# Kernel tuning notes

Hardware: AMD Instinct MI355X
Metric: run time of the kernel (lower is better)

Reference implementation:

```python
import jax, jax.numpy as jnp
import numpy as np

B, S, CA, CS, CZ, H, L, N = 1, 1024, 768, 384, 64, 16, 2, 2
C = CA // H  # head dim = 48


def setup_inputs():
    key = jax.random.key(0)
    ks = iter(jax.random.split(key, 40))

    def w(shape, scale=0.02):
        return jax.random.normal(next(ks), shape, jnp.float32) * scale

    return dict(
        a=jax.random.normal(next(ks), (B, S, CA), jnp.float32),
        s=jax.random.normal(next(ks), (B, S, CS), jnp.float32),
        z=jax.random.normal(next(ks), (B, S, S, CZ), jnp.float32),
        attn_sn_w=jnp.ones((L, CS), jnp.float32),
        attn_pb_w=w((L, CA, CS)), attn_pb_b=jnp.zeros((L, CA), jnp.float32),
        attn_pnb_w=w((L, CA, CS)),
        pair_w=jnp.ones((L, CZ), jnp.float32), pair_b=jnp.zeros((L, CZ), jnp.float32),
        q_w=w((L, CA, CA)), q_b=jnp.zeros((L, CA), jnp.float32),
        kvg_w=w((L, 3 * CA, CA)),
        bias_w=w((L, H, CZ)), bias_b=jnp.zeros((L, H), jnp.float32),
        ao_w=w((L, CA, CA)),
        out_w=w((L, CA, CS)), out_b=jnp.full((L, CA), -2.0, jnp.float32),
        tr_sn_w=jnp.ones((L, CS), jnp.float32),
        tr_pb_w=w((L, CA, CS)), tr_pb_b=jnp.zeros((L, CA), jnp.float32),
        tr_pnb_w=w((L, CA, CS)),
        tr_a_w=w((L, 2 * N * CA, CA)),
        tr_s_w=w((L, CA, CS)), tr_s_b=jnp.full((L, CA), -2.0, jnp.float32),
        tr_b_w=w((L, CA, N * CA)),
    )


def _ln(x, w=None, b=None, eps=1e-5):
    m = jnp.mean(x, -1, keepdims=True)
    v = jnp.mean(jnp.square(x - m), -1, keepdims=True)
    y = (x - m) * jax.lax.rsqrt(v + eps)
    if w is not None:
        y = y * w
    if b is not None:
        y = y + b
    return y


def _adaln(a, s, sn_w, pb_w, pb_b, pnb_w):
    an = _ln(a)        # LayerNorm, no affine
    sn = _ln(s, sn_w)  # LayerNorm, weight only (bias=False)
    # NOTE: sigmoid wraps the ENTIRE expression, as in the torch source.
    return jax.nn.sigmoid((sn @ pb_w.T + pb_b) * an + sn @ pnb_w.T)


def _forward(a, s, z, attn_sn_w, attn_pb_w, attn_pb_b, attn_pnb_w,
             pair_w, pair_b, q_w, q_b, kvg_w, bias_w, bias_b, ao_w,
             out_w, out_b, tr_sn_w, tr_pb_w, tr_pb_b, tr_pnb_w,
             tr_a_w, tr_s_w, tr_s_b, tr_b_w):
    for l in range(L):
        # ---- AttentionPairBias (beta = 0, s is not None) ----
        a2 = _adaln(a, s, attn_sn_w[l], attn_pb_w[l], attn_pb_b[l], attn_pnb_w[l])
        # torch uses a raw .reshape((B, H, S, c)) with NO transpose -> replicate exactly
        q = (a2 @ q_w[l].T + q_b[l]).reshape(B, H, S, C)
        kvg = (a2 @ kvg_w[l].T).reshape(B, H, S, 3 * C)
        k, v, g = jnp.split(kvg, 3, axis=-1)
        bmat = (_ln(z, pair_w[l], pair_b[l]) @ bias_w[l].T + bias_b[l]).reshape(B, H, S, S)
        scores = jnp.einsum('bhic,bhjc->bhji', q, k) / C + bmat  # divide by c, NOT sqrt(c)
        A = jax.nn.softmax(scores, axis=-1)
        o = jnp.einsum('bhij,bhic->bhjc', A, v)
        attn = (jax.nn.sigmoid(g) * o).reshape(B, S, CA) @ ao_w[l].T
        attn = jax.nn.sigmoid(s @ out_w[l].T + out_b[l]) * attn
        # ---- ConditionedTransitionBlock ----
        a3 = _adaln(a, s, tr_sn_w[l], tr_pb_w[l], tr_pb_b[l], tr_pnb_w[l])
        h1, h2 = jnp.split(a3 @ tr_a_w[l].T, 2, axis=-1)
        bb = jax.nn.silu(h1) * h2
        tr = jax.nn.sigmoid((s @ tr_s_w[l].T + tr_s_b[l]) * (bb @ tr_b_w[l].T))
        a = attn + tr
    return a


def reference(a, s, z, attn_sn_w, attn_pb_w, attn_pb_b, attn_pnb_w,
              pair_w, pair_b, q_w, q_b, kvg_w, bias_w, bias_b, ao_w,
              out_w, out_b, tr_sn_w, tr_pb_w, tr_pb_b, tr_pnb_w,
              tr_a_w, tr_s_w, tr_s_b, tr_b_w):
    return _forward(a, s, z, attn_sn_w, attn_pb_w, attn_pb_b, attn_pnb_w,
                    pair_w, pair_b, q_w, q_b, kvg_w, bias_w, bias_b, ao_w,
                    out_w, out_b, tr_sn_w, tr_pb_w, tr_pb_b, tr_pnb_w,
                    tr_a_w, tr_s_w, tr_s_b, tr_b_w)
```

## Files before the change

kernel.cpp:

```cpp
#include <hip/hip_runtime.h>
#include <hip/hip_bf16.h>
#include <hip/hip_fp16.h>

typedef long long i64;
typedef unsigned short u16;
typedef __attribute__((ext_vector_type(8))) short short8;
typedef __attribute__((ext_vector_type(8))) _Float16 half8;
typedef __attribute__((ext_vector_type(4))) float f32x4;

__device__ __forceinline__ float sigf(float x){ return 1.f/(1.f + __expf(-x)); }
__device__ __forceinline__ u16 f2bu(float v){
  union{ __hip_bfloat16 h; u16 u; } cv; cv.h = __float2bfloat16(v); return cv.u;
}
__device__ __forceinline__ u16 f2hu(float v){
  union{ _Float16 h; u16 u; } cv; cv.h = (_Float16)v; return cv.u;
}
__device__ __forceinline__ float h2f(u16 u){
  union{ u16 u; _Float16 h; } cv; cv.u = u; return (float)cv.h;
}

__global__ void f2b(const float* __restrict__ in, u16* __restrict__ outp, long n){
  long i = ((long)blockIdx.x*256 + threadIdx.x)*4;
  if (i < n){
    float4 v = *(const float4*)(in + i);
    outp[i]   = f2bu(v.x); outp[i+1] = f2bu(v.y);
    outp[i+2] = f2bu(v.z); outp[i+3] = f2bu(v.w);
  }
}

__global__ void f2b_wpool(const float* __restrict__ w0, const float* __restrict__ w1,
                          const float* __restrict__ w2, const float* __restrict__ w3,
                          const float* __restrict__ w4, const float* __restrict__ w5,
                          const float* __restrict__ w6, const float* __restrict__ w7,
                          const float* __restrict__ w8, const float* __restrict__ w9,
                          const float* __restrict__ w10, u16* __restrict__ pool){
  long i = ((long)blockIdx.x*256 + threadIdx.x)*4;
  if (i >= 8257536) return;
  const float* src; long rel;
  if      (i <  294912){ src=w0;  rel=i; }
  else if (i <  589824){ src=w1;  rel=i-294912; }
  else if (i < 1179648){ src=w2;  rel=i-589824; }
  else if (i < 2949120){ src=w3;  rel=i-1179648; }
  else if (i < 3538944){ src=w4;  rel=i-2949120; }
  else if (i < 3833856){ src=w5;  rel=i-3538944; }
  else if (i < 4128768){ src=w6;  rel=i-3833856; }
  else if (i < 4423680){ src=w7;  rel=i-4128768; }
  else if (i < 4718592){ src=w8;  rel=i-4423680; }
  else if (i < 7077888){ src=w9;  rel=i-4718592; }
  else                 { src=w10; rel=i-7077888; }
  float4 v = *(const float4*)(src + rel);
  pool[i]   = f2bu(v.x); pool[i+1] = f2bu(v.y);
  pool[i+2] = f2bu(v.z); pool[i+3] = f2bu(v.w);
}

__global__ __launch_bounds__(256) void ln_rows(const float* __restrict__ x,
                                               float* __restrict__ y, int D){
  long base = (long)blockIdx.x * D;
  int t = threadIdx.x;
  float s = 0.f, ss = 0.f;
  for (int i = t; i < D; i += 256){ float v = x[base+i]; s += v; ss += v*v; }
  __shared__ float r0[256], r1[256];
  r0[t] = s; r1[t] = ss; __syncthreads();
  for (int off = 128; off > 0; off >>= 1){
    if (t < off){ r0[t] += r0[t+off]; r1[t] += r1[t+off]; }
    __syncthreads();
  }
  float mean = r0[0]/D;
  float var  = r1[0]/D - mean*mean;
  float rstd = rsqrtf(var + 1e-5f);
  for (int i = t; i < D; i += 256) y[base+i] = (x[base+i]-mean)*rstd;
}

__global__ void scale2(const float* __restrict__ SN0, const float* __restrict__ w_at,
                       const float* __restrict__ w_tr, u16* __restrict__ y){
  long i = (long)blockIdx.x*256 + threadIdx.x;
  if (i < 786432){
    long tt = i/768, c = i%768;
    float v = (c < 384) ? SN0[tt*384+c]*w_at[c] : SN0[tt*384+c-384]*w_tr[c-384];
    y[i] = f2bu(v);
  }
}

__global__ void adaln2(const float* __restrict__ Pf, const float* __restrict__ AN,
                       const float* __restrict__ b, u16* __restrict__ outb){
  long i = (long)blockIdx.x*256 + threadIdx.x;
  if (i < 786432){
    long tt = i/768, c = i%768;
    float p1 = Pf[tt*1536 + c] + b[c];
    float p2 = Pf[tt*1536 + 768 + c];
    outb[i] = f2bu(sigf(p1*AN[i] + p2));
  }
}

__global__ void catbias(const float* __restrict__ ob, const float* __restrict__ tb,
                        float* __restrict__ g){
  int i = blockIdx.x*256 + threadIdx.x;
  if (i < 3072){
    int l = i/1536, c = i%1536;
    g[i] = (c < 768) ? ob[l*768+c] : tb[l*768+c-768];
  }
}

__global__ void zprep(const float* __restrict__ pw, const float* __restrict__ pb,
                      const float* __restrict__ bw, const float* __restrict__ bb,
                      u16* __restrict__ cwh, float* __restrict__ cb){
  int i = blockIdx.x*256 + threadIdx.x;
  if (i < 2048){
    int l = i/1024, c = i%64;
    cwh[i] = f2hu(pw[l*64+c]*bw[i]);
  } else if (i < 2080){
    int t = i - 2048;
    int l = t/16, mm = t%16;
    float acc = bb[l*16+mm];
    for (int c = 0; c < 64; c++) acc += pb[l*64+c]*bw[l*1024+mm*64+c];
    cb[t] = acc;
  }
}

__global__ __launch_bounds__(256) void zln_mfma(const float* __restrict__ z,
    const u16* __restrict__ Bw,
    const float* __restrict__ cb,
    u16* __restrict__ Zp){
  __shared__ __align__(16) u16 Asm[256*72];
  __shared__ __align__(16) u16 Bsm[32*72];
  int t = threadIdx.x;
  i64 p0 = (i64)blockIdx.x*256;
  if (t < 64){
    int row = t >> 1, half = t & 1;
    const uint4* src = (const uint4*)(Bw + row*64 + half*32);
    uint4* dst = (uint4*)&Bsm[row*72 + half*32];
    dst[0]=src[0]; dst[1]=src[1]; dst[2]=src[2]; dst[3]=src[3];
  }
  int sub = t & 15, rbase = t >> 4;
  const float* zb = z + p0*64;
#pragma unroll
  for (int it = 0; it < 16; it++){
    int row = it*16 + rbase;
    float4 v = *(const float4*)(zb + (i64)row*64 + sub*4);
    float s  = v.x+v.y+v.z+v.w;
    float ss = v.x*v.x+v.y*v.y+v.z*v.z+v.w*v.w;
#pragma unroll
    for (int mk = 1; mk < 16; mk <<= 1){
      s  += __shfl_xor(s,  mk);
      ss += __shfl_xor(ss, mk);
    }
    float mean = s*(1.f/64.f);
    float var  = ss*(1.f/64.f) - mean*mean;
    float r = rsqrtf(var + 1e-5f);
    unsigned int lo = (unsigned int)f2hu((v.x-mean)*r) | ((unsigned int)f2hu((v.y-mean)*r) << 16);
    unsigned int hi = (unsigned int)f2hu((v.z-mean)*r) | ((unsigned int)f2hu((v.w-mean)*r) << 16);
    *(uint2*)&Asm[row*72 + sub*4] = make_uint2(lo, hi);
  }
  __syncthreads();
  int lane = t & 63, wv = t >> 6, la = lane & 15, quad = lane >> 4;
  f32x4 acc[4][2] = {};
#pragma unroll
  for (int kc = 0; kc < 2; kc++){
    half8 af[4], bf[2];
#pragma unroll
    for (int i = 0; i < 4; i++)
      af[i] = *(const half8*)&Asm[(64*wv + 16*i + la)*72 + kc*32 + quad*8];
#pragma unroll
    for (int j = 0; j < 2; j++)
      bf[j] = *(const half8*)&Bsm[(16*j + la)*72 + kc*32 + quad*8];
#pragma unroll
    for (int i = 0; i < 4; i++)
#pragma unroll
      for (int j = 0; j < 2; j++)
        acc[i][j] = __builtin_amdgcn_mfma_f32_16x16x32_f16(af[i], bf[j], acc[i][j], 0,0,0);
  }
  __syncthreads();
#pragma unroll
  for (int i = 0; i < 4; i++)
#pragma unroll
   for (int j = 0; j < 2; j++)
#pragma unroll
    for (int rr = 0; rr < 4; rr++){
      int row = 64*wv + 16*i + quad*4 + rr;
      int gn = 16*j + la;
      Asm[row*72 + gn] = f2hu(acc[i][j][rr] + cb[gn]);
    }
  __syncthreads();
  uint4* o0 = (uint4*)(Zp + (p0 + t)*16);
  uint4* o1 = (uint4*)(Zp + 16777216 + (p0 + t)*16);
  o0[0] = *(uint4*)&Asm[t*72];
  o0[1] = *(uint4*)&Asm[t*72 + 8];
  o1[0] = *(uint4*)&Asm[t*72 + 16];
  o1[1] = *(uint4*)&Asm[t*72 + 24];
}

__global__ __launch_bounds__(256) void rowstat(const float* __restrict__ sc,
                                               float2* __restrict__ st){
  long base = (long)blockIdx.x * 1024;
  const float4* row = (const float4*)(sc + base);
  int t = threadIdx.x;
  float4 v = row[t];
  float mx = fmaxf(fmaxf(v.x,v.y), fmaxf(v.z,v.w));
  for (int off = 32; off > 0; off >>= 1) mx = fmaxf(mx, __shfl_down(mx, off));
  __shared__ float sm[4], ssum[4];
  int wv = t >> 6, ln = t & 63;
  if (ln == 0) sm[wv] = mx;
  __syncthreads();
  mx = fmaxf(fmaxf(sm[0],sm[1]), fmaxf(sm[2],sm[3]));
  float s = __expf(v.x-mx)+__expf(v.y-mx)+__expf(v.z-mx)+__expf(v.w-mx);
  for (int off = 32; off > 0; off >>= 1) s += __shfl_down(s, off);
  if (ln == 0) ssum[wv] = s;
  __syncthreads();
  if (t == 0) st[blockIdx.x] = make_float2(mx, 1.f/(ssum[0]+ssum[1]+ssum[2]+ssum[3]));
}

__global__ __launch_bounds__(256) void vtrans(const float* __restrict__ kvg,
                                              u16* __restrict__ vt){
  int h = blockIdx.x, x0 = blockIdx.y*64;
  __shared__ u16 tile[48][65];
  int t = threadIdx.x;
  for (int idx = t; idx < 64*48; idx += 256){
    int xx = idx/48, c = idx%48;
    tile[c][xx] = f2hu(kvg[(i64)h*147456 + (i64)(x0+xx)*144 + 48 + c]);
  }
  __syncthreads();
  for (int idx = t; idx < 48*64; idx += 256){
    int c = idx>>6, xx = idx&63;
    vt[(i64)h*49152 + (i64)c*1024 + x0 + xx] = tile[c][xx];
  }
}

__global__ __launch_bounds__(256) void av_gemm(
    const float* __restrict__ P,
    const float2* __restrict__ st,
    const u16* __restrict__ Vt,
    const float* __restrict__ kvg,
    u16* __restrict__ Ob)
{
  __shared__ __align__(16) u16 Asm[64*40];
  __shared__ __align__(16) u16 Bsm[64*40];
  int t = threadIdx.x;
  int h = blockIdx.z;
  int m0 = blockIdx.y*64;
  const float* Pp = P + (i64)h*1048576;
  const float2* stp = st + (i64)h*1024;
  const u16* Vp = Vt + (i64)h*49152;
  int lane = t & 63, wv = t >> 6;
  int la = lane & 15, quad = lane >> 4;
  int moff = (wv >> 1)*32, noff = (wv & 1)*32;
  int mcol = t & 63;
  int kr0  = (t >> 6)*2;
  int srow = t >> 2, skc = (t & 3)*8;
  f32x4 acc[2][2] = {{{0.f,0.f,0.f,0.f},{0.f,0.f,0.f,0.f}},
                     {{0.f,0.f,0.f,0.f},{0.f,0.f,0.f,0.f}}};
  float va[4], vb[4];
  float2 sa[4], sb[4];
  uint4 bv;
#pragma unroll
  for (int q = 0; q < 4; q++){
    int kk = kr0 + q*8;
    sa[q] = stp[kk]; sb[q] = stp[kk+1];
    va[q] = Pp[(i64)kk*1024 + m0 + mcol];
    vb[q] = Pp[(i64)(kk+1)*1024 + m0 + mcol];
  }
  bv = make_uint4(0,0,0,0);
  if (srow < 48) bv = *(const uint4*)(Vp + (i64)srow*1024 + skc);
  for (int it = 0; it < 32; it++){
#pragma unroll
    for (int q = 0; q < 4; q++){
      int kk = kr0 + q*8;
      unsigned int pa = f2hu(__expf(va[q] - sa[q].x) * sa[q].y);
      unsigned int pb = f2hu(__expf(vb[q] - sb[q].x) * sb[q].y);
      *(unsigned int*)&Asm[mcol*40 + kk] = pa | (pb << 16);
    }
    *(uint4*)&Bsm[srow*40 + skc] = bv;
    __syncthreads();
    if (it < 31){
      int k0 = (it+1)*32;
#pragma unroll
      for (int q = 0; q < 4; q++){
        int kk = kr0 + q*8;
        sa[q] = stp[k0+kk]; sb[q] = stp[k0+kk+1];
        va[q] = Pp[(i64)(k0+kk)*1024 + m0 + mcol];
        vb[q] = Pp[(i64)(k0+kk+1)*1024 + m0 + mcol];
      }
      bv = make_uint4(0,0,0,0);
      if (srow < 48) bv = *(const uint4*)(Vp + (i64)srow*1024 + k0 + skc);
    }
    half8 af0 = *(const half8*)&Asm[(moff      + la)*40 + quad*8];
    half8 af1 = *(const half8*)&Asm[(moff + 16 + la)*40 + quad*8];
    half8 bf0 = *(const half8*)&Bsm[(noff      + la)*40 + quad*8];
    half8 bf1 = *(const half8*)&Bsm[(noff + 16 + la)*40 + quad*8];
    acc[0][0] = __builtin_amdgcn_mfma_f32_16x16x32_f16(af0, bf0, acc[0][0], 0,0,0);
    acc[0][1] = __builtin_amdgcn_mfma_f32_16x16x32_f16(af0, bf1, acc[0][1], 0,0,0);
    acc[1][0] = __builtin_amdgcn_mfma_f32_16x16x32_f16(af1, bf0, acc[1][0], 0,0,0);
    acc[1][1] = __builtin_amdgcn_mfma_f32_16x16x32_f16(af1, bf1, acc[1][1], 0,0,0);
    __syncthreads();
  }
#pragma unroll
  for (int i = 0; i < 2; i++)
#pragma unroll
   for (int j = 0; j < 2; j++)
#pragma unroll
    for (int r = 0; r < 4; r++){
      int gm = m0 + moff + 16*i + quad*4 + r;
      int gn = noff + 16*j + la;
      if (gn < 48){
        float g = kvg[(i64)h*147456 + (i64)gm*144 + 96 + gn];
        float v = sigf(g) * acc[i][j][r];
        Ob[(i64)h*49152 + (i64)gm*48 + gn] = f2bu(v);
      }
    }
}

__global__ void silu_mul_bf(const float* __restrict__ h, u16* __restrict__ bb, long n){
  long i = (long)blockIdx.x*256 + threadIdx.x;
  if (i < n){
    long tt = i/1536, c = i%1536;
    float h1 = h[tt*3072 + c], h2 = h[tt*3072 + 1536 + c];
    bb[i] = f2bu(h1*sigf(h1)*h2);
  }
}

template<int EPI>
__global__ __launch_bounds__(256) void gbt(
    const u16* __restrict__ A, i64 lda, i64 sbA,
    const u16* __restrict__ B, i64 ldb, i64 sbB,
    float* __restrict__ C, i64 ldc, i64 sbC,
    u16* __restrict__ Cbf,
    const float* __restrict__ bias,
    const void* __restrict__ X1, const void* __restrict__ X2,
    float* __restrict__ C2,
    int K, float alpha)
{
  __shared__ __align__(16) u16 Asm[64*72];
  __shared__ __align__(16) u16 Bsm[64*72];
  int t = threadIdx.x;
  int bz = blockIdx.z;
  int m0 = blockIdx.y*64, n0 = blockIdx.x*64;
  int srow = t >> 2, skc = (t & 3)*16;
  const u16* Ar = A + (i64)bz*sbA + (i64)(m0+srow)*lda;
  const u16* Br = B + (i64)bz*sbB + (i64)(n0+srow)*ldb;
  int lane = t & 63, wv = t >> 6;
  int la = lane & 15, quad = lane >> 4;
  int moff = (wv >> 1)*32, noff = (wv & 1)*32;
  f32x4 acc[2][2] = {{{0.f,0.f,0.f,0.f},{0.f,0.f,0.f,0.f}},
                     {{0.f,0.f,0.f,0.f},{0.f,0.f,0.f,0.f}}};
  for (int k0 = 0; k0 < K; k0 += 64){
    uint4 av0 = make_uint4(0,0,0,0), av1 = av0, bv0 = av0, bv1 = av0;
    if (k0 + skc < K){
      av0 = *(const uint4*)(Ar + k0 + skc);
      bv0 = *(const uint4*)(Br + k0 + skc);
    }
    if (k0 + skc + 8 < K){
      av1 = *(const uint4*)(Ar + k0 + skc + 8);
      bv1 = *(const uint4*)(Br + k0 + skc + 8);
    }
    *(uint4*)&Asm[srow*72 + skc]     = av0;
    *(uint4*)&Asm[srow*72 + skc + 8] = av1;
    *(uint4*)&Bsm[srow*72 + skc]     = bv0;
    *(uint4*)&Bsm[srow*72 + skc + 8] = bv1;
    __syncthreads();
#pragma unroll
    for (int kc = 0; kc < 2; kc++){
      short8 af0 = *(const short8*)&Asm[(moff      + la)*72 + kc*32 + quad*8];
      short8 af1 = *(const short8*)&Asm[(moff + 16 + la)*72 + kc*32 + quad*8];
      short8 bf0 = *(const short8*)&Bsm[(noff      + la)*72 + kc*32 + quad*8];
      short8 bf1 = *(const short8*)&Bsm[(noff + 16 + la)*72 + kc*32 + quad*8];
      acc[0][0] = __builtin_amdgcn_mfma_f32_16x16x32_bf16(af0, bf0, acc[0][0], 0,0,0);
      acc[0][1] = __builtin_amdgcn_mfma_f32_16x16x32_bf16(af0, bf1, acc[0][1], 0,0,0);
      acc[1][0] = __builtin_amdgcn_mfma_f32_16x16x32_bf16(af1, bf0, acc[1][0], 0,0,0);
      acc[1][1] = __builtin_amdgcn_mfma_f32_16x16x32_bf16(af1, bf1, acc[1][1], 0,0,0);
    }
    __syncthreads();
  }
  float* Cb = C ? C + (i64)bz*sbC : nullptr;
  u16* Cb2 = Cbf ? Cbf + (i64)bz*sbC : nullptr;
  const u16* zp = (EPI == 1) ? (const u16*)X1 + (i64)bz*sbC : nullptr;
#pragma unroll
  for (int i = 0; i < 2; i++)
#pragma unroll
   for (int j = 0; j < 2; j++)
#pragma unroll
    for (int r = 0; r < 4; r++){
      int gm = m0 + moff + 16*i + quad*4 + r;
      int gn = n0 + noff + 16*j + la;
      i64 idx = (i64)gm*ldc + gn;
      float v = acc[i][j][r];
      if (EPI == 1){
        Cb[idx] = alpha*v + h2f(zp[idx]);
      } else if (EPI == 3){
        const float* g = (const float*)X1;
        Cb[idx] = sigf(g[(i64)gm*1536 + gn]) * v;
      } else if (EPI == 4){
        const float* am = (const float*)X1;
        const float* sg = (const float*)X2;
        float res = am[(i64)gm*768 + gn] + sigf(sg[(i64)gm*1536 + gn] * v);
        Cb[idx] = res;
        if (C2) C2[idx] = res;
      } else {
        if (bias) v += bias[gn];
        if (Cb)  Cb[idx]  = v;
        if (Cb2) Cb2[idx] = f2bu(v);
      }
    }
}

extern "C" void kernel_launch(void* const* d_in, const int* in_sizes, int n_in,
                              void* d_out, int out_size, void* d_ws, size_t ws_size,
                              hipStream_t stream){
  const float* a_in   = (const float*)d_in[0];
  const float* s_in   = (const float*)d_in[1];
  const float* z_in   = (const float*)d_in[2];
  const float* attn_sn_w = (const float*)d_in[3];
  const float* attn_pb_w = (const float*)d_in[4];
  const float* attn_pb_b = (const float*)d_in[5];
  const float* attn_pnb_w= (const float*)d_in[6];
  const float* pair_w = (const float*)d_in[7];
  const float* pair_b = (const float*)d_in[8];
  const float* q_w    = (const float*)d_in[9];
  const float* q_b    = (const float*)d_in[10];
  const float* kvg_w  = (const float*)d_in[11];
  const float* bias_w = (const float*)d_in[12];
  const float* bias_b = (const float*)d_in[13];
  const float* ao_w   = (const float*)d_in[14];
  const float* out_w  = (const float*)d_in[15];
  const float* out_b  = (const float*)d_in[16];
  const float* tr_sn_w= (const float*)d_in[17];
  const float* tr_pb_w= (const float*)d_in[18];
  const float* tr_pb_b= (const float*)d_in[19];
  const float* tr_pnb_w=(const float*)d_in[20];
  const float* tr_a_w = (const float*)d_in[21];
  const float* tr_s_w = (const float*)d_in[22];
  const float* tr_s_b = (const float*)d_in[23];
  const float* tr_b_w = (const float*)d_in[24];

  float* ws      = (float*)d_ws;
  float* scores  = ws;
  float* hbuf    = scores;
  float* gfused  = scores + 3145728;
  float* attnmm  = scores + 4718592;
  float* a_cur   = ws + 16777216;
  float* AN      = a_cur + 786432;
  float* SN0     = AN + 786432;
  float* Pfused  = SN0 + 393216;
  float* kvg     = Pfused + 1572864;
  float* vaux    = kvg + 2359296;
  float* gbias   = vaux + 786432;
  float* zcw     = gbias + 3072;
  float* zcb     = zcw + 2048;
  u16* wpool     = (u16*)(zcb + 64);
  u16* SNw2_bf   = wpool + 8257536;
  u16* s_bf      = SNw2_bf + 786432;
  u16* a2bf      = s_bf + 393216;
  u16* qproj_bf  = a2bf + 786432;
  u16* kvg_bf    = qproj_bf + 786432;
  u16* ogated_bf = kvg_bf + 2359296;
  u16* bbuf_bf   = ogated_bf + 786432;
  u16* Zp2       = bbuf_bf + 1572864;

  u16*    Vt_h   = (u16*)vaux;
  float2* rstats = (float2*)(vaux + 393216);
  u16*    zcwh   = (u16*)zcw;

  const i64 OFF_PB=0, OFF_Q=589824, OFF_KVG=1179648, OFF_AO=2949120,
            OFF_OUT=3538944, OFF_TPB=4128768, OFF_TRA=4718592, OFF_TRB=7077888;

  f2b<<<384,256,0,stream>>>(s_in, s_bf, 393216);
  ln_rows<<<1024,256,0,stream>>>(s_in, SN0, 384);
  catbias<<<12,256,0,stream>>>(out_b, tr_s_b, gbias);
  zprep<<<9,256,0,stream>>>(pair_w, pair_b, bias_w, bias_b, zcwh, zcb);
  zln_mfma<<<4096,256,0,stream>>>(z_in, zcwh, zcb, Zp2);

  for (int l = 0; l < 2; l++){
    f2b_wpool<<<8064,256,0,stream>>>(
        attn_pb_w + (i64)l*294912, attn_pnb_w + (i64)l*294912,
        q_w + (i64)l*589824, kvg_w + (i64)l*1769472, ao_w + (i64)l*589824,
        out_w + (i64)l*294912, tr_s_w + (i64)l*294912,
        tr_pb_w + (i64)l*294912, tr_pnb_w + (i64)l*294912,
        tr_a_w + (i64)l*2359296, tr_b_w + (i64)l*1179648, wpool);

    ln_rows<<<1024,256,0,stream>>>(l == 0 ? a_in : a_cur, AN, 768);
    scale2<<<3072,256,0,stream>>>(SN0, attn_sn_w + l*384, tr_sn_w + l*384, SNw2_bf);

    gbt<0><<<dim3(24,16,1),256,0,stream>>>(SNw2_bf,768,0, wpool+OFF_PB,384,0,
        Pfused,1536,0, nullptr, nullptr, nullptr, nullptr, nullptr, 384, 1.f);
    adaln2<<<3072,256,0,stream>>>(Pfused, AN, attn_pb_b + l*768, a2bf);

    gbt<0><<<dim3(12,16,1),256,0,stream>>>(a2bf,768,0, wpool+OFF_Q,768,0,
        nullptr,768,0, qproj_bf, q_b + l*768, nullptr, nullptr, nullptr, 768, 1.f);
    gbt<0><<<dim3(36,16,1),256,0,stream>>>(a2bf,768,0, wpool+OFF_KVG,768,0,
        kvg,2304,0, kvg_bf, nullptr, nullptr, nullptr, nullptr, 768, 1.f);

    gbt<1><<<dim3(16,16,16),256,0,stream>>>(kvg_bf,144,147456, qproj_bf,48,49152,
        scores,1024,1048576, nullptr, nullptr, Zp2 + (i64)l*16777216, nullptr, nullptr,
        48, 1.f/48.f);

    rowstat<<<16384,256,0,stream>>>(scores, rstats);
    vtrans<<<dim3(16,16),256,0,stream>>>(kvg, Vt_h);
    av_gemm<<<dim3(1,16,16),256,0,stream>>>(scores, rstats, Vt_h, kvg, ogated_bf);

    gbt<0><<<dim3(24,16,1),256,0,stream>>>(s_bf,384,0, wpool+OFF_OUT,384,0,
        gfused,1536,0, nullptr, gbias + l*1536, nullptr, nullptr, nullptr, 384, 1.f);

    gbt<3><<<dim3(12,16,1),256,0,stream>>>(ogated_bf,768,0, wpool+OFF_AO,768,0,
        attnmm,768,0, nullptr, nullptr, gfused, nullptr, nullptr, 768, 1.f);

    gbt<0><<<dim3(24,16,1),256,0,stream>>>(SNw2_bf+384,768,0, wpool+OFF_TPB,384,0,
        Pfused,1536,0, nullptr, nullptr, nullptr, nullptr, nullptr, 384, 1.f);
    adaln2<<<3072,256,0,stream>>>(Pfused, AN, tr_pb_b + l*768, a2bf);

    gbt<0><<<dim3(48,16,1),256,0,stream>>>(a2bf,768,0, wpool+OFF_TRA,768,0,
        hbuf,3072,0, nullptr, nullptr, nullptr, nullptr, nullptr, 768, 1.f);
    silu_mul_bf<<<6144,256,0,stream>>>(hbuf, bbuf_bf, 1572864);

    gbt<4><<<dim3(12,16,1),256,0,stream>>>(bbuf_bf,1536,0, wpool+OFF_TRB,1536,0,
        a_cur,768,0, nullptr, nullptr, attnmm, gfused + 768,
        (l==1) ? (float*)d_out : nullptr, 1536, 1.f);
  }
}
```

Baseline: 865.3 us.

## Fuse softmax row stats into score GEMM and batch layer-independent work

The score GEMM epilogue now computes per-tile row max and sum-of-exp partials, and a small merge kernel combines them. This replaces the separate rowstat pass, which re-read the full 16x1024x1024 score tensor. Layer-independent work (weight conversion for both layers, the s-only AdaLN projections and output gates) is hoisted out of the layer loop into batched launches, and the Q and KVG projections are merged into one GEMM with a split epilogue. The cost is more workspace and a heavier GEMM epilogue with shuffles and a shared-memory sync.

```diff
diff --git a/kernel.cpp b/kernel.cpp
--- a/kernel.cpp
+++ b/kernel.cpp
@@ -7,6 +7,8 @@
 typedef __attribute__((ext_vector_type(8))) short short8;
 typedef __attribute__((ext_vector_type(8))) _Float16 half8;
 typedef __attribute__((ext_vector_type(4))) float f32x4;
+
+#define POOLSZ 8257536
 
 __device__ __forceinline__ float sigf(float x){ return 1.f/(1.f + __expf(-x)); }
 __device__ __forceinline__ u16 f2bu(float v){
@@ -35,20 +37,22 @@
                           const float* __restrict__ w8, const float* __restrict__ w9,
                           const float* __restrict__ w10, u16* __restrict__ pool){
   long i = ((long)blockIdx.x*256 + threadIdx.x)*4;
-  if (i >= 8257536) return;
-  const float* src; long rel;
-  if      (i <  294912){ src=w0;  rel=i; }
-  else if (i <  589824){ src=w1;  rel=i-294912; }
-  else if (i < 1179648){ src=w2;  rel=i-589824; }
-  else if (i < 2949120){ src=w3;  rel=i-1179648; }
-  else if (i < 3538944){ src=w4;  rel=i-2949120; }
-  else if (i < 3833856){ src=w5;  rel=i-3538944; }
-  else if (i < 4128768){ src=w6;  rel=i-3833856; }
-  else if (i < 4423680){ src=w7;  rel=i-4128768; }
-  else if (i < 4718592){ src=w8;  rel=i-4423680; }
-  else if (i < 7077888){ src=w9;  rel=i-4718592; }
-  else                 { src=w10; rel=i-7077888; }
-  float4 v = *(const float4*)(src + rel);
+  if (i >= 2L*POOLSZ) return;
+  long l = i / POOLSZ;
+  long j = i - l*POOLSZ;
+  const float* src; long rel, ls;
+  if      (j <  294912){ src=w0;  rel=j;          ls=294912; }
+  else if (j <  589824){ src=w1;  rel=j-294912;   ls=294912; }
+  else if (j < 1179648){ src=w2;  rel=j-589824;   ls=589824; }
+  else if (j < 2949120){ src=w3;  rel=j-1179648;  ls=1769472; }
+  else if (j < 3538944){ src=w4;  rel=j-2949120;  ls=589824; }
+  else if (j < 3833856){ src=w5;  rel=j-3538944;  ls=294912; }
+  else if (j < 4128768){ src=w6;  rel=j-3833856;  ls=294912; }
+  else if (j < 4423680){ src=w7;  rel=j-4128768;  ls=294912; }
+  else if (j < 4718592){ src=w8;  rel=j-4423680;  ls=294912; }
+  else if (j < 7077888){ src=w9;  rel=j-4718592;  ls=2359296; }
+  else                 { src=w10; rel=j-7077888;  ls=1179648; }
+  float4 v = *(const float4*)(src + l*ls + rel);
   pool[i]   = f2bu(v.x); pool[i+1] = f2bu(v.y);
   pool[i+2] = f2bu(v.z); pool[i+3] = f2bu(v.w);
 }
@@ -71,12 +75,13 @@
   for (int i = t; i < D; i += 256) y[base+i] = (x[base+i]-mean)*rstd;
 }
 
-__global__ void scale2(const float* __restrict__ SN0, const float* __restrict__ w_at,
-                       const float* __restrict__ w_tr, u16* __restrict__ y){
+__global__ void scale2(const float* __restrict__ SN0, const float* __restrict__ at_w,
+                       const float* __restrict__ tr_w, u16* __restrict__ y){
   long i = (long)blockIdx.x*256 + threadIdx.x;
-  if (i < 786432){
-    long tt = i/768, c = i%768;
-    float v = (c < 384) ? SN0[tt*384+c]*w_at[c] : SN0[tt*384+c-384]*w_tr[c-384];
+  if (i < 1572864){
+    long l = i / 786432, j = i - l*786432;
+    long tt = j/768, c = j%768;
+    float v = (c < 384) ? SN0[tt*384+c]*at_w[l*384+c] : SN0[tt*384+c-384]*tr_w[l*384+c-384];
     y[i] = f2bu(v);
   }
 }
@@ -92,35 +97,31 @@
   }
 }
 
-__global__ void catbias(const float* __restrict__ ob, const float* __restrict__ tb,
-                        float* __restrict__ g){
+__global__ void prep_small(const float* __restrict__ ob, const float* __restrict__ tb,
+                           float* __restrict__ g,
+                           const float* __restrict__ pw, const float* __restrict__ pb,
+                           const float* __restrict__ bw, const float* __restrict__ bb,
+                           u16* __restrict__ cwh, float* __restrict__ cb){
   int i = blockIdx.x*256 + threadIdx.x;
   if (i < 3072){
     int l = i/1536, c = i%1536;
     g[i] = (c < 768) ? ob[l*768+c] : tb[l*768+c-768];
   }
-}
-
-__global__ void zprep(const float* __restrict__ pw, const float* __restrict__ pb,
-                      const float* __restrict__ bw, const float* __restrict__ bb,
-                      u16* __restrict__ cwh, float* __restrict__ cb){
-  int i = blockIdx.x*256 + threadIdx.x;
-  if (i < 2048){
-    int l = i/1024, c = i%64;
-    cwh[i] = f2hu(pw[l*64+c]*bw[i]);
-  } else if (i < 2080){
-    int t = i - 2048;
-    int l = t/16, mm = t%16;
+  int j = i - 3072;
+  if (j >= 0 && j < 2048){
+    int l = j/1024, c = j%64;
+    cwh[j] = f2hu(pw[l*64+c]*bw[j]);
+  } else if (j >= 2048 && j < 2080){
+    int t2 = j - 2048;
+    int l = t2/16, mm = t2%16;
     float acc = bb[l*16+mm];
     for (int c = 0; c < 64; c++) acc += pb[l*64+c]*bw[l*1024+mm*64+c];
-    cb[t] = acc;
+    cb[t2] = acc;
   }
 }
 
 __global__ __launch_bounds__(256) void zln_mfma(const float* __restrict__ z,
-    const u16* __restrict__ Bw,
-    const float* __restrict__ cb,
-    u16* __restrict__ Zp){
+    const u16* __restrict__ Bw, const float* __restrict__ cb, u16* __restrict__ Zp){
   __shared__ __align__(16) u16 Asm[256*72];
   __shared__ __align__(16) u16 Bsm[32*72];
   int t = threadIdx.x;
@@ -189,24 +190,23 @@
   o1[1] = *(uint4*)&Asm[t*72 + 24];
 }
 
-__global__ __launch_bounds__(256) void rowstat(const float* __restrict__ sc,
-                                               float2* __restrict__ st){
-  long base = (long)blockIdx.x * 1024;
-  const float4* row = (const float4*)(sc + base);
-  int t = threadIdx.x;
-  float4 v = row[t];
-  float mx = fmaxf(fmaxf(v.x,v.y), fmaxf(v.z,v.w));
-  for (int off = 32; off > 0; off >>= 1) mx = fmaxf(mx, __shfl_down(mx, off));
-  __shared__ float sm[4], ssum[4];
-  int wv = t >> 6, ln = t & 63;
-  if (ln == 0) sm[wv] = mx;
-  __syncthreads();
-  mx = fmaxf(fmaxf(sm[0],sm[1]), fmaxf(sm[2],sm[3]));
-  float s = __expf(v.x-mx)+__expf(v.y-mx)+__expf(v.z-mx)+__expf(v.w-mx);
-  for (int off = 32; off > 0; off >>= 1) s += __shfl_down(s, off);
-  if (ln == 0) ssum[wv] = s;
-  __syncthreads();
-  if (t == 0) st[blockIdx.x] = make_float2(mx, 1.f/(ssum[0]+ssum[1]+ssum[2]+ssum[3]));
+__global__ __launch_bounds__(256) void stat_merge(const float2* __restrict__ pt,
+                                                  float2* __restrict__ st){
+  int i = blockIdx.x*256 + threadIdx.x;
+  int h = i >> 10, k = i & 1023;
+  const float2* p = pt + (i64)h*16384 + k;
+  float mx[16], sm[16];
+  float m = -3e38f;
+#pragma unroll
+  for (int nb = 0; nb < 16; nb++){
+    float2 v = p[(i64)nb*1024];
+    mx[nb] = v.x; sm[nb] = v.y;
+    m = fmaxf(m, v.x);
+  }
+  float s = 0.f;
+#pragma unroll
+  for (int nb = 0; nb < 16; nb++) s += sm[nb]*__expf(mx[nb]-m);
+  st[i] = make_float2(m, 1.f/s);
 }
 
 __global__ __launch_bounds__(256) void vtrans(const float* __restrict__ kvg,
@@ -226,10 +226,8 @@
 }
 
 __global__ __launch_bounds__(256) void av_gemm(
-    const float* __restrict__ P,
-    const float2* __restrict__ st,
-    const u16* __restrict__ Vt,
-    const float* __restrict__ kvg,
+    const float* __restrict__ P, const float2* __restrict__ st,
+    const u16* __restrict__ Vt, const float* __restrict__ kvg,
     u16* __restrict__ Ob)
 {
   __shared__ __align__(16) u16 Asm[64*40];
@@ -323,13 +321,14 @@
     const u16* __restrict__ B, i64 ldb, i64 sbB,
     float* __restrict__ C, i64 ldc, i64 sbC,
     u16* __restrict__ Cbf,
-    const float* __restrict__ bias,
+    const float* __restrict__ bias, i64 sbBias,
     const void* __restrict__ X1, const void* __restrict__ X2,
     float* __restrict__ C2,
     int K, float alpha)
 {
   __shared__ __align__(16) u16 Asm[64*72];
   __shared__ __align__(16) u16 Bsm[64*72];
+  __shared__ float2 pst[2][64];
   int t = threadIdx.x;
   int bz = blockIdx.z;
   int m0 = blockIdx.y*64, n0 = blockIdx.x*64;
@@ -371,7 +370,64 @@
   }
   float* Cb = C ? C + (i64)bz*sbC : nullptr;
   u16* Cb2 = Cbf ? Cbf + (i64)bz*sbC : nullptr;
-  const u16* zp = (EPI == 1) ? (const u16*)X1 + (i64)bz*sbC : nullptr;
+  if (EPI == 1){
+    const u16* zp = (const u16*)X1 + (i64)bz*sbC;
+    float vv[2][2][4], rmax[2][4], rsum[2][4];
+#pragma unroll
+    for (int i = 0; i < 2; i++)
+#pragma unroll
+     for (int r = 0; r < 4; r++){ rmax[i][r] = -3e38f; rsum[i][r] = 0.f; }
+#pragma unroll
+    for (int i = 0; i < 2; i++)
+#pragma unroll
+     for (int j = 0; j < 2; j++)
+#pragma unroll
+      for (int r = 0; r < 4; r++){
+        int gm = m0 + moff + 16*i + quad*4 + r;
+        int gn = n0 + noff + 16*j + la;
+        i64 idx = (i64)gm*ldc + gn;
+        float v = alpha*acc[i][j][r] + h2f(zp[idx]);
+        Cb[idx] = v;
+        vv[i][j][r] = v;
+        rmax[i][r] = fmaxf(rmax[i][r], v);
+      }
+#pragma unroll
+    for (int mk = 1; mk < 16; mk <<= 1)
+#pragma unroll
+      for (int i = 0; i < 2; i++)
+#pragma unroll
+       for (int r = 0; r < 4; r++)
+        rmax[i][r] = fmaxf(rmax[i][r], __shfl_xor(rmax[i][r], mk));
+#pragma unroll
+    for (int i = 0; i < 2; i++)
+#pragma unroll
+     for (int j = 0; j < 2; j++)
+#pragma unroll
+      for (int r = 0; r < 4; r++)
+        rsum[i][r] += __expf(vv[i][j][r] - rmax[i][r]);
+#pragma unroll
+    for (int mk = 1; mk < 16; mk <<= 1)
+#pragma unroll
+      for (int i = 0; i < 2; i++)
+#pragma unroll
+       for (int r = 0; r < 4; r++)
+        rsum[i][r] += __shfl_xor(rsum[i][r], mk);
+    if (la == 0){
+#pragma unroll
+      for (int i = 0; i < 2; i++)
+#pragma unroll
+       for (int r = 0; r < 4; r++)
+        pst[wv & 1][moff + 16*i + quad*4 + r] = make_float2(rmax[i][r], rsum[i][r]);
+    }
+    __syncthreads();
+    if (t < 64){
+      float2 pa = pst[0][t], pb = pst[1][t];
+      float m = fmaxf(pa.x, pb.x);
+      float s = pa.y*__expf(pa.x-m) + pb.y*__expf(pb.x-m);
+      ((float2*)C2)[((i64)bz*16 + blockIdx.x)*1024 + m0 + t] = make_float2(m, s);
+    }
+    return;
+  }
 #pragma unroll
   for (int i = 0; i < 2; i++)
 #pragma unroll
@@ -382,9 +438,7 @@
       int gn = n0 + noff + 16*j + la;
       i64 idx = (i64)gm*ldc + gn;
       float v = acc[i][j][r];
-      if (EPI == 1){
-        Cb[idx] = alpha*v + h2f(zp[idx]);
-      } else if (EPI == 3){
+      if (EPI == 3){
         const float* g = (const float*)X1;
         Cb[idx] = sigf(g[(i64)gm*1536 + gn]) * v;
       } else if (EPI == 4){
@@ -393,8 +447,17 @@
         float res = am[(i64)gm*768 + gn] + sigf(sg[(i64)gm*1536 + gn] * v);
         Cb[idx] = res;
         if (C2) C2[idx] = res;
+      } else if (EPI == 5){
+        u16* qp = (u16*)C2;
+        if (gn < 768){
+          qp[(i64)gm*768 + gn] = f2bu(v + bias[gn]);
+        } else {
+          i64 ix = (i64)gm*2304 + (gn - 768);
+          Cb[ix]  = v;
+          Cb2[ix] = f2bu(v);
+        }
       } else {
-        if (bias) v += bias[gn];
+        if (bias) v += bias[(i64)bz*sbBias + gn];
         if (Cb)  Cb[idx]  = v;
         if (Cb2) Cb2[idx] = f2bu(v);
       }
@@ -433,84 +496,74 @@
   float* ws      = (float*)d_ws;
   float* scores  = ws;
   float* hbuf    = scores;
-  float* gfused  = scores + 3145728;
-  float* attnmm  = scores + 4718592;
   float* a_cur   = ws + 16777216;
   float* AN      = a_cur + 786432;
   float* SN0     = AN + 786432;
-  float* Pfused  = SN0 + 393216;
-  float* kvg     = Pfused + 1572864;
-  float* vaux    = kvg + 2359296;
-  float* gbias   = vaux + 786432;
-  float* zcw     = gbias + 3072;
-  float* zcb     = zcw + 2048;
-  u16* wpool     = (u16*)(zcb + 64);
-  u16* SNw2_bf   = wpool + 8257536;
-  u16* s_bf      = SNw2_bf + 786432;
+  float* kvg     = SN0 + 393216;
+  float* attnmm  = kvg + 2359296;
+  float* Pf_at   = attnmm + 786432;
+  float* Pf_tr   = Pf_at + 3145728;
+  float* gfused2 = Pf_tr + 3145728;
+  float2* partials = (float2*)(gfused2 + 3145728);
+  float2* rstats   = (float2*)((float*)partials + 1048576);
+  float* gbias   = (float*)rstats + 32768;
+  u16*   zcwh    = (u16*)(gbias + 3072);
+  float* zcb     = gbias + 3072 + 1024;
+  u16* wpool2    = (u16*)(zcb + 64);
+  u16* SNw2      = wpool2 + 16515072;
+  u16* s_bf      = SNw2 + 1572864;
   u16* a2bf      = s_bf + 393216;
   u16* qproj_bf  = a2bf + 786432;
   u16* kvg_bf    = qproj_bf + 786432;
   u16* ogated_bf = kvg_bf + 2359296;
   u16* bbuf_bf   = ogated_bf + 786432;
   u16* Zp2       = bbuf_bf + 1572864;
-
-  u16*    Vt_h   = (u16*)vaux;
-  float2* rstats = (float2*)(vaux + 393216);
-  u16*    zcwh   = (u16*)zcw;
-
-  const i64 OFF_PB=0, OFF_Q=589824, OFF_KVG=1179648, OFF_AO=2949120,
+  u16* Vt_h      = Zp2 + 33554432;
+
+  const i64 OFF_PB=0, OFF_Q=589824, OFF_AO=2949120,
             OFF_OUT=3538944, OFF_TPB=4128768, OFF_TRA=4718592, OFF_TRB=7077888;
 
   f2b<<<384,256,0,stream>>>(s_in, s_bf, 393216);
   ln_rows<<<1024,256,0,stream>>>(s_in, SN0, 384);
-  catbias<<<12,256,0,stream>>>(out_b, tr_s_b, gbias);
-  zprep<<<9,256,0,stream>>>(pair_w, pair_b, bias_w, bias_b, zcwh, zcb);
+  prep_small<<<21,256,0,stream>>>(out_b, tr_s_b, gbias,
+      pair_w, pair_b, bias_w, bias_b, zcwh, zcb);
   zln_mfma<<<4096,256,0,stream>>>(z_in, zcwh, zcb, Zp2);
+  f2b_wpool<<<16128,256,0,stream>>>(attn_pb_w, attn_pnb_w, q_w, kvg_w, ao_w,
+      out_w, tr_s_w, tr_pb_w, tr_pnb_w, tr_a_w, tr_b_w, wpool2);
+  scale2<<<6144,256,0,stream>>>(SN0, attn_sn_w, tr_sn_w, SNw2);
+  gbt<0><<<dim3(24,16,2),256,0,stream>>>(SNw2,768,786432, wpool2+OFF_PB,384,POOLSZ,
+      Pf_at,1536,1572864, nullptr, nullptr,0, nullptr,nullptr,nullptr, 384,1.f);
+  gbt<0><<<dim3(24,16,2),256,0,stream>>>(SNw2+384,768,786432, wpool2+OFF_TPB,384,POOLSZ,
+      Pf_tr,1536,1572864, nullptr, nullptr,0, nullptr,nullptr,nullptr, 384,1.f);
+  gbt<0><<<dim3(24,16,2),256,0,stream>>>(s_bf,384,0, wpool2+OFF_OUT,384,POOLSZ,
+      gfused2,1536,1572864, nullptr, gbias,1536, nullptr,nullptr,nullptr, 384,1.f);
 
   for (int l = 0; l < 2; l++){
-    f2b_wpool<<<8064,256,0,stream>>>(
-        attn_pb_w + (i64)l*294912, attn_pnb_w + (i64)l*294912,
-        q_w + (i64)l*589824, kvg_w + (i64)l*1769472, ao_w + (i64)l*589824,
-        out_w + (i64)l*294912, tr_s_w + (i64)l*294912,
-        tr_pb_w + (i64)l*294912, tr_pnb_w + (i64)l*294912,
-        tr_a_w + (i64)l*2359296, tr_b_w + (i64)l*1179648, wpool);
-
+    const u16* wp = wpool2 + (i64)l*POOLSZ;
     ln_rows<<<1024,256,0,stream>>>(l == 0 ? a_in : a_cur, AN, 768);
-    scale2<<<3072,256,0,stream>>>(SN0, attn_sn_w + l*384, tr_sn_w + l*384, SNw2_bf);
-
-    gbt<0><<<dim3(24,16,1),256,0,stream>>>(SNw2_bf,768,0, wpool+OFF_PB,384,0,
-        Pfused,1536,0, nullptr, nullptr, nullptr, nullptr, nullptr, 384, 1.f);
-    adaln2<<<3072,256,0,stream>>>(Pfused, AN, attn_pb_b + l*768, a2bf);
-
-    gbt<0><<<dim3(12,16,1),256,0,stream>>>(a2bf,768,0, wpool+OFF_Q,768,0,
-        nullptr,768,0, qproj_bf, q_b + l*768, nullptr, nullptr, nullptr, 768, 1.f);
-    gbt<0><<<dim3(36,16,1),256,0,stream>>>(a2bf,768,0, wpool+OFF_KVG,768,0,
-        kvg,2304,0, kvg_bf, nullptr, nullptr, nullptr, nullptr, 768, 1.f);
+    adaln2<<<3072,256,0,stream>>>(Pf_at + (i64)l*1572864, AN, attn_pb_b + l*768, a2bf);
+
+    gbt<5><<<dim3(48,16,1),256,0,stream>>>(a2bf,768,0, wp+OFF_Q,768,0,
+        kvg,2304,0, kvg_bf, q_b + l*768,0, nullptr,nullptr, (float*)qproj_bf, 768,1.f);
 
     gbt<1><<<dim3(16,16,16),256,0,stream>>>(kvg_bf,144,147456, qproj_bf,48,49152,
-        scores,1024,1048576, nullptr, nullptr, Zp2 + (i64)l*16777216, nullptr, nullptr,
-        48, 1.f/48.f);
-
-    rowstat<<<16384,256,0,stream>>>(scores, rstats);
+        scores,1024,1048576, nullptr, nullptr,0, Zp2 + (i64)l*16777216, nullptr,
+        (float*)partials, 48, 1.f/48.f);
+    stat_merge<<<64,256,0,stream>>>(partials, rstats);
+
     vtrans<<<dim3(16,16),256,0,stream>>>(kvg, Vt_h);
     av_gemm<<<dim3(1,16,16),256,0,stream>>>(scores, rstats, Vt_h, kvg, ogated_bf);
 
-    gbt<0><<<dim3(24,16,1),256,0,stream>>>(s_bf,384,0, wpool+OFF_OUT,384,0,
-        gfused,1536,0, nullptr, gbias + l*1536, nullptr, nullptr, nullptr, 384, 1.f);
-
-    gbt<3><<<dim3(12,16,1),256,0,stream>>>(ogated_bf,768,0, wpool+OFF_AO,768,0,
-        attnmm,768,0, nullptr, nullptr, gfused, nullptr, nullptr, 768, 1.f);
-
-    gbt<0><<<dim3(24,16,1),256,0,stream>>>(SNw2_bf+384,768,0, wpool+OFF_TPB,384,0,
-        Pfused,1536,0, nullptr, nullptr, nullptr, nullptr, nullptr, 384, 1.f);
-    adaln2<<<3072,256,0,stream>>>(Pfused, AN, tr_pb_b + l*768, a2bf);
-
-    gbt<0><<<dim3(48,16,1),256,0,stream>>>(a2bf,768,0, wpool+OFF_TRA,768,0,
-        hbuf,3072,0, nullptr, nullptr, nullptr, nullptr, nullptr, 768, 1.f);
+    gbt<3><<<dim3(12,16,1),256,0,stream>>>(ogated_bf,768,0, wp+OFF_AO,768,0,
+        attnmm,768,0, nullptr, nullptr,0, gfused2 + (i64)l*1572864, nullptr,nullptr, 768,1.f);
+
+    adaln2<<<3072,256,0,stream>>>(Pf_tr + (i64)l*1572864, AN, tr_pb_b + l*768, a2bf);
+    gbt<0><<<dim3(48,16,1),256,0,stream>>>(a2bf,768,0, wp+OFF_TRA,768,0,
+        hbuf,3072,0, nullptr, nullptr,0, nullptr,nullptr,nullptr, 768,1.f);
     silu_mul_bf<<<6144,256,0,stream>>>(hbuf, bbuf_bf, 1572864);
 
-    gbt<4><<<dim3(12,16,1),256,0,stream>>>(bbuf_bf,1536,0, wpool+OFF_TRB,1536,0,
-        a_cur,768,0, nullptr, nullptr, attnmm, gfused + 768,
-        (l==1) ? (float*)d_out : nullptr, 1536, 1.f);
-  }
-}
+    gbt<4><<<dim3(12,16,1),256,0,stream>>>(bbuf_bf,1536,0, wp+OFF_TRB,1536,0,
+        a_cur,768,0, nullptr, nullptr,0, attnmm, gfused2 + (i64)l*1572864 + 768,
+        (l==1) ? (float*)d_out : nullptr, 1536,1.f);
+  }
+}
```

Result: faster. 800.3 us (-7.5%).
